# Performance work log

Measured on AMD Instinct MI355X. Metric: run time of the kernel, lower is better.

## Reference

```python
import jax, jax.numpy as jnp
import numpy as np

WAY, SHOT, QUERY, T, DIM, SEM, NCLS, HW = 20, 5, 50, 8, 640, 300, 351, 11
TEMP = 0.5


def l2n(x, axis=-1, eps=1e-12):
    n = jnp.sqrt(jnp.sum(x * x, axis=axis, keepdims=True))
    return x / jnp.maximum(n, eps)


def lrelu(x):
    return jnp.where(x >= 0, x, 0.1 * x)


def setup_inputs() -> dict:
    key = jax.random.key(0)
    ks = jax.random.split(key, 12)
    std = np.sqrt(2.0 / DIM).astype(np.float32)
    return {
        'spt': jax.random.normal(ks[0], (SHOT * WAY, DIM, HW, HW), jnp.float32),
        'qry': jax.random.normal(ks[1], (QUERY * WAY, DIM, HW, HW), jnp.float32),
        'label2vec': jax.random.normal(ks[2], (WAY, SEM), jnp.float32),
        'w1': jax.random.normal(ks[3], (T, SEM, SEM), jnp.float32) * 0.02,
        'b1': jnp.zeros((T, SEM), jnp.float32),
        'w2': jax.random.normal(ks[4], (T, DIM, SEM), jnp.float32) * 0.02,
        'b2': jnp.zeros((T, DIM), jnp.float32),
        'weight_base': jax.random.normal(ks[5], (NCLS, T, DIM), jnp.float32) * std,
        'wq': jnp.broadcast_to(jnp.eye(DIM, dtype=jnp.float32), (T, DIM, DIM)) + jax.random.normal(ks[6], (T, DIM, DIM), jnp.float32) * 0.001,
        'bq': jnp.zeros((T, DIM), jnp.float32),
        'wkeys': jax.random.normal(ks[7], (T, NCLS, DIM), jnp.float32) * std,
        'scale_att': jnp.full((T,), 10.0, jnp.float32),
        'lamda_novel': jnp.ones((T,), jnp.float32),
        'lamda_base': jnp.ones((T,), jnp.float32),
        'wt1': jax.random.normal(ks[8], (SEM // 2, SEM), jnp.float32) * 0.02,
        'bt1': jnp.zeros((SEM // 2,), jnp.float32),
        'wt2': jax.random.normal(ks[9], (T, SEM // 2), jnp.float32) * 0.02,
        'bt2': jnp.zeros((T,), jnp.float32),
        'templet_bias': jnp.zeros((T,), jnp.float32),
        'tl1': jnp.ones((1,), jnp.float32),
        'tl2': jnp.ones((1,), jnp.float32),
    }


def reference(spt, qry, label2vec, w1, b1, w2, b2, weight_base, wq, bq, wkeys,
              scale_att, lamda_novel, lamda_base, wt1, bt1, wt2, bt2,
              templet_bias, tl1, tl2):
    spt_f = spt.reshape(SHOT, WAY, DIM, HW, HW)
    # per-template semantic MLP -> 1x1 conv filters [T, way, DIM]
    h = lrelu(jnp.einsum('ws,tds->twd', label2vec, w1) + b1[:, None, :])
    filt = jnp.einsum('twd,tcd->twc', h, w2) + b2[:, None, :]
    # mean_normalize = L2 normalize along channel dim
    spt_n = l2n(spt_f, axis=2)
    qry_n = l2n(qry, axis=1)
    filt_n = l2n(filt, axis=-1)
    # support: sigmoid attention maps (1x1 conv), spatially-normalized pooling
    act_s = jax.nn.sigmoid(jnp.einsum('swcxy,twc->swtxy', spt_n, filt_n))
    act_s = act_s / jnp.sum(act_s, axis=(-1, -2), keepdims=True)
    spt_t = jnp.einsum('swcxy,swtxy->swtc', spt_n, act_s)   # [shot,way,T,D]
    spt_tn = l2n(spt_t, axis=-1)
    # attention-based weight transfer from base classes (eval: all classes)
    wb_n = l2n(weight_base, axis=-1)                        # [K,T,D]
    qe = l2n(jnp.einsum('swtc,tdc->swtd', spt_tn, wq) + bq[None, None], axis=-1)
    wk_n = l2n(wkeys, axis=-1)                              # [T,K,D]
    att = jax.nn.softmax(scale_att[None, None, :, None] * jnp.einsum('swtd,tkd->swtk', qe, wk_n), axis=-1)
    wtb = jnp.einsum('swtk,ktd->swtd', att, wb_n)           # [shot,way,T,D]
    lam_n = (lamda_novel ** 2)[None, None, :, None]
    lam_b = (lamda_base ** 2)[None, None, :, None]
    comb = lam_n * spt_tn + lam_b * wtb
    proto = l2n(jnp.mean(comb, axis=0, keepdims=True), axis=-1)  # [1,way,T,D]
    # query: per-way attention maps and pooling
    act_q = jax.nn.sigmoid(jnp.einsum('qcxy,twc->wqtxy', qry_n, filt_n))
    act_q = act_q / jnp.sum(act_q, axis=(-1, -2), keepdims=True)
    qry_t = jnp.einsum('qcxy,wqtxy->wqtc', qry_n, act_q)    # [way,Q,T,D]
    qry_tn = l2n(qry_t, axis=-1)
    # per-template similarity: einsum('mikl,ijkl->mjik').mean(0) -> [Q,way,T]
    sim = jnp.mean(jnp.einsum('mikd,ijkd->mjik', proto, qry_tn), axis=0)
    # semantic template weights
    h2 = lrelu(label2vec @ wt1.T + bt1)
    wgt = jax.nn.sigmoid(h2 @ wt2.T + bt2)                  # [way,T]
    wgt = (tl1 ** 2) * jax.nn.sigmoid(templet_bias) + (tl2 ** 2) * wgt
    wgt = wgt / jnp.sum(wgt, axis=-1, keepdims=True)
    logits = jnp.sum(sim * wgt[None], axis=-1)              # [Q,way]
    return logits / TEMP
```

## Files before the change

### kernel.cpp

```cpp
#include <hip/hip_runtime.h>
#include <hip/hip_bf16.h>

#define NWAY 20
#define NSHOT 5
#define NT 8
#define NDIM 640
#define NSEM 300
#define NSEMH 150
#define NCLS 351
#define NXY 121
#define NWT 160

typedef short s16x8 __attribute__((ext_vector_type(8)));
typedef float f32x4 __attribute__((ext_vector_type(4)));
typedef float f32x4u __attribute__((ext_vector_type(4), aligned(4)));

__device__ __forceinline__ float sigmoidf_(float x) { return 1.0f / (1.0f + expf(-x)); }
__device__ __forceinline__ float lreluf_(float x) { return x >= 0.0f ? x : 0.1f * x; }
__device__ __forceinline__ float invl2_(float ss) { return 1.0f / fmaxf(sqrtf(ss), 1e-12f); }

__device__ __forceinline__ unsigned bfr_(float f) {
    unsigned b = __float_as_uint(f);
    return (b + 0x7FFFu + ((b >> 16) & 1u)) >> 16;
}
__device__ __forceinline__ unsigned pkbf_(float a, float b) { return bfr_(a) | (bfr_(b) << 16); }

__device__ __forceinline__ s16x8 cvt8_(const float* p) {
    f32x4u a = *(const f32x4u*)p;
    f32x4u b = *(const f32x4u*)(p + 4);
    union { unsigned u[4]; s16x8 v; } r;
    r.u[0] = pkbf_(a[0], a[1]); r.u[1] = pkbf_(a[2], a[3]);
    r.u[2] = pkbf_(b[0], b[1]); r.u[3] = pkbf_(b[2], b[3]);
    return r.v;
}

__device__ __forceinline__ float waveReduceSum(float v) {
#pragma unroll
    for (int off = 32; off > 0; off >>= 1) v += __shfl_down(v, off, 64);
    return v;
}

__global__ __launch_bounds__(256) void k_prepw(const float* __restrict__ l2v,
    const float* __restrict__ w1, const float* __restrict__ b1,
    const float* __restrict__ w2, const float* __restrict__ b2,
    const float* __restrict__ wq, const float* __restrict__ wk,
    const float* __restrict__ wb, const float* __restrict__ wt1,
    const float* __restrict__ bt1, const float* __restrict__ wt2,
    const float* __restrict__ bt2, const float* __restrict__ tb,
    const float* __restrict__ tl1, const float* __restrict__ tl2,
    ushort* __restrict__ filtb, float* __restrict__ wgt,
    unsigned* __restrict__ wqb_u, ushort* __restrict__ wknb,
    float* __restrict__ invb)
{
    int b = blockIdx.x;
    int tid = threadIdx.x, lane = tid & 63, wv = tid >> 6;
    __shared__ float red4[4];
    __shared__ float l2s[NSEM];
    __shared__ float hS[NSEM];
    __shared__ float fS[NDIM];
    __shared__ float h2[NSEMH];
    __shared__ float wl[NT];
    __shared__ float ssum;

    if (b < 1600) {
        size_t i = ((size_t)b * 256 + tid) * 8;
        const f32x4u a = *(const f32x4u*)(wq + i);
        const f32x4u c = *(const f32x4u*)(wq + i + 4);
        wqb_u[i / 2 + 0] = pkbf_(a[0], a[1]);
        wqb_u[i / 2 + 1] = pkbf_(a[2], a[3]);
        wqb_u[i / 2 + 2] = pkbf_(c[0], c[1]);
        wqb_u[i / 2 + 3] = pkbf_(c[2], c[3]);
        return;
    }
    if (b < 4408) {
        int r = b - 1600;
        int t = r / NCLS, k = r - t * NCLS;
        const float* src = wk + (size_t)r * NDIM;
        float v0 = src[tid], v1 = src[tid + 256];
        bool h = tid < 128;
        float v2 = h ? src[tid + 512] : 0.f;
        float ss = v0 * v0 + v1 * v1 + v2 * v2;
        ss = waveReduceSum(ss);
        if (lane == 0) red4[wv] = ss;
        __syncthreads();
        float inv = invl2_(red4[0] + red4[1] + red4[2] + red4[3]);
        ushort* dst = wknb + ((size_t)t * 384 + k) * NDIM;
        dst[tid] = (ushort)bfr_(v0 * inv);
        dst[tid + 256] = (ushort)bfr_(v1 * inv);
        if (h) dst[tid + 512] = (ushort)bfr_(v2 * inv);
        return;
    }
    if (b < 7216) {
        int r = b - 4408;
        const float* src = wb + (size_t)r * NDIM;
        float v0 = src[tid], v1 = src[tid + 256];
        float v2 = (tid < 128) ? src[tid + 512] : 0.f;
        float ss = v0 * v0 + v1 * v1 + v2 * v2;
        ss = waveReduceSum(ss);
        if (lane == 0) red4[wv] = ss;
        __syncthreads();
        if (tid == 0) invb[r] = invl2_(red4[0] + red4[1] + red4[2] + red4[3]);
        return;
    }
    if (b < 7376) {
        int wt = b - 7216;
        int w = wt >> 3, t = wt & 7;
        for (int s = tid; s < NSEM; s += 256) l2s[s] = l2v[w * NSEM + s];
        __syncthreads();
        for (int d = tid; d < NSEM; d += 256) {
            const f32x4u* wr = (const f32x4u*)(w1 + ((size_t)t * NSEM + d) * NSEM);
            float a0 = 0.f, a1 = 0.f, a2 = 0.f, a3 = 0.f;
#pragma unroll 5
            for (int s4 = 0; s4 < 75; ++s4) {
                f32x4u v = wr[s4];
                a0 += v[0] * l2s[s4 * 4 + 0];
                a1 += v[1] * l2s[s4 * 4 + 1];
                a2 += v[2] * l2s[s4 * 4 + 2];
                a3 += v[3] * l2s[s4 * 4 + 3];
            }
            hS[d] = lreluf_((a0 + a1) + (a2 + a3) + b1[t * NSEM + d]);
        }
        __syncthreads();
        for (int c = tid; c < NDIM; c += 256) {
            const f32x4u* wr = (const f32x4u*)(w2 + ((size_t)t * NDIM + c) * NSEM);
            float a0 = 0.f, a1 = 0.f, a2 = 0.f, a3 = 0.f;
#pragma unroll 5
            for (int s4 = 0; s4 < 75; ++s4) {
                f32x4u v = wr[s4];
                a0 += v[0] * hS[s4 * 4 + 0];
                a1 += v[1] * hS[s4 * 4 + 1];
                a2 += v[2] * hS[s4 * 4 + 2];
                a3 += v[3] * hS[s4 * 4 + 3];
            }
            fS[c] = (a0 + a1) + (a2 + a3) + b2[t * NDIM + c];
        }
        __syncthreads();
        float ss = 0.f;
        for (int c = tid; c < NDIM; c += 256) ss += fS[c] * fS[c];
        ss = waveReduceSum(ss);
        if (lane == 0) red4[wv] = ss;
        __syncthreads();
        float inv = invl2_(red4[0] + red4[1] + red4[2] + red4[3]);
        for (int c = tid; c < NDIM; c += 256)
            filtb[(size_t)wt * NDIM + c] = (ushort)bfr_(fS[c] * inv);
        return;
    }
    {
        int w = b - 7376;
        if (tid < NSEMH) {
            float acc = 0.f;
            for (int s = 0; s < NSEM; ++s) acc += l2v[w * NSEM + s] * wt1[tid * NSEM + s];
            h2[tid] = lreluf_(acc + bt1[tid]);
        }
        __syncthreads();
        if (tid < NT) {
            float acc = 0.f;
            for (int d = 0; d < NSEMH; ++d) acc += h2[d] * wt2[tid * NSEMH + d];
            float wg = sigmoidf_(acc + bt2[tid]);
            wl[tid] = tl1[0] * tl1[0] * sigmoidf_(tb[tid]) + tl2[0] * tl2[0] * wg;
        }
        __syncthreads();
        if (tid == 0) { float s2 = 0.f; for (int t = 0; t < NT; ++t) s2 += wl[t]; ssum = s2; }
        __syncthreads();
        if (tid < NT) wgt[w * NT + tid] = wl[tid] / ssum;
    }
}

__global__ __launch_bounds__(256) void k_wbT(const float* __restrict__ wb,
    const float* __restrict__ invb, unsigned* __restrict__ wbnT_u)
{
    int k0 = blockIdx.x * 64, c0 = blockIdx.y * 64, t = blockIdx.z;
    int tid = threadIdx.x;
    __shared__ float tile[64][65];
    __shared__ float invT[64];
    {
        int i = tid >> 2, q = tid & 3;
        int kg = min(k0 + i, NCLS - 1);
#pragma unroll
        for (int u = 0; u < 4; ++u) {
            int c = q * 16 + u * 4;
            f32x4u v = *(const f32x4u*)(wb + ((size_t)kg * NT + t) * NDIM + c0 + c);
            tile[i][c] = v[0]; tile[i][c + 1] = v[1]; tile[i][c + 2] = v[2]; tile[i][c + 3] = v[3];
        }
        if (tid < 64) {
            int kg2 = k0 + tid;
            invT[tid] = (kg2 < NCLS) ? invb[(size_t)kg2 * NT + t] : 0.f;
        }
    }
    __syncthreads();
    int cc = tid >> 2, qq = tid & 3;
    size_t rowo = (((size_t)t * NDIM + c0 + cc) * 384 + k0) / 2;
#pragma unroll
    for (int u = 0; u < 8; ++u) {
        int kl = qq * 16 + u * 2;
        float v0 = tile[kl][cc] * invT[kl];
        float v1 = tile[kl + 1][cc] * invT[kl + 1];
        wbnT_u[rowo + qq * 8 + u] = pkbf_(v0, v1);
    }
}

__global__ __launch_bounds__(512) void k_support2(const float* __restrict__ spt,
    const ushort* __restrict__ filtb, float* __restrict__ sptn,
    ushort* __restrict__ xb)
{
    int w = blockIdx.x, s = blockIdx.y;
    int n = s * NWAY + w;
    int tid = threadIdx.x, lane = tid & 63, wv = tid >> 6;
    int l15 = lane & 15, lh = lane >> 4;
    const float* base = spt + (size_t)n * NDIM * NXY;

    __shared__ unsigned actL[16 * 64];
    __shared__ float redT[8 * 8];
    __shared__ float invt[8];

    for (int i = tid; i < 16 * 64; i += 512) actL[i] = 0u;

    int xy = wv * 16 + l15;
    const float* colb = base + (xy < NXY ? xy : 0);
    const ushort* arow1 = filtb + (size_t)(w * NT + (l15 & 7)) * NDIM + lh * 8;
    f32x4 acc = {0.f, 0.f, 0.f, 0.f};
    float ssq = 0.f;
    for (int c0 = 0; c0 < NDIM; c0 += 32) {
        float v[8];
#pragma unroll
        for (int j = 0; j < 8; ++j) {
            v[j] = colb[(size_t)(c0 + lh * 8 + j) * NXY];
            ssq += v[j] * v[j];
        }
        union { unsigned u[4]; s16x8 x; } bf;
#pragma unroll
        for (int p = 0; p < 4; ++p) bf.u[p] = pkbf_(v[2 * p], v[2 * p + 1]);
        s16x8 af = *(const s16x8*)(arow1 + c0);
        acc = __builtin_amdgcn_mfma_f32_16x16x32_bf16(af, bf.x, acc, 0, 0, 0);
    }
    ssq += __shfl_xor(ssq, 16, 64);
    ssq += __shfl_xor(ssq, 32, 64);
    float inv = (xy < NXY) ? invl2_(ssq) : 0.f;
    __syncthreads();
#pragma unroll
    for (int r = 0; r < 4; ++r) {
        int row = lh * 4 + r;
        if (row < 8) {
            float a = sigmoidf_(acc[r] * inv) * inv;
            unsigned g = ((unsigned)(xy >> 3) ^ (unsigned)row) & 15u;
            *(ushort*)((char*)actL + (size_t)row * 256 + g * 16 + (xy & 7) * 2) = (ushort)bfr_(a);
        }
    }
    __syncthreads();

    f32x4 acc2[5];
#pragma unroll
    for (int f = 0; f < 5; ++f) acc2[f] = (f32x4){0.f, 0.f, 0.f, 0.f};
#pragma unroll
    for (int ks = 0; ks < 4; ++ks) {
        int xyb = ks * 32 + lh * 8;
        unsigned g = ((unsigned)(ks * 4 + lh) ^ (unsigned)l15) & 15u;
        s16x8 af = *(const s16x8*)&actL[l15 * 64 + g * 4];
#pragma unroll
        for (int f = 0; f < 5; ++f) {
            int c = (wv * 5 + f) * 16 + l15;
            const float* rp = base + (size_t)c * NXY;
            s16x8 bfv;
            if (ks == 3 && lh == 3) {
                union { unsigned u[4]; s16x8 v; } r;
                r.u[0] = pkbf_(rp[120], 0.f); r.u[1] = 0u; r.u[2] = 0u; r.u[3] = 0u;
                bfv = r.v;
            } else {
                bfv = cvt8_(rp + xyb);
            }
            acc2[f] = __builtin_amdgcn_mfma_f32_16x16x32_bf16(af, bfv, acc2[f], 0, 0, 0);
        }
    }
    {
        float pr[4] = {0.f, 0.f, 0.f, 0.f};
#pragma unroll
        for (int f = 0; f < 5; ++f)
#pragma unroll
            for (int r = 0; r < 4; ++r) pr[r] += acc2[f][r] * acc2[f][r];
#pragma unroll
        for (int r = 0; r < 4; ++r) {
#pragma unroll
            for (int off = 1; off < 16; off <<= 1) pr[r] += __shfl_xor(pr[r], off, 64);
        }
        if (l15 == 0 && lh < 2) {
#pragma unroll
            for (int r = 0; r < 4; ++r) redT[wv * 8 + lh * 4 + r] = pr[r];
        }
    }
    __syncthreads();
    if (tid < 8) {
        float s8 = 0.f;
#pragma unroll
        for (int w8 = 0; w8 < 8; ++w8) s8 += redT[w8 * 8 + tid];
        invt[tid] = invl2_(s8);
    }
    __syncthreads();
    if (lh < 2) {
#pragma unroll
        for (int f = 0; f < 5; ++f) {
            int c = (wv * 5 + f) * 16 + l15;
#pragma unroll
            for (int r = 0; r < 4; ++r) {
                int t = lh * 4 + r;
                float val = acc2[f][r] * invt[t];
                sptn[((size_t)n * NT + t) * NDIM + c] = val;
                xb[((size_t)t * 112 + n) * NDIM + c] = (ushort)bfr_(val);
            }
        }
    }
}

__global__ __launch_bounds__(512) void k_qatt(const ushort* __restrict__ xb,
    const ushort* __restrict__ wqb, const float* __restrict__ bq,
    const ushort* __restrict__ wknb, const ushort* __restrict__ wbnT,
    const float* __restrict__ sptn, const float* __restrict__ scale_att,
    const float* __restrict__ lamn, const float* __restrict__ lamb,
    float* __restrict__ comb)
{
    int t = blockIdx.x, mt = blockIdx.y, n0 = mt * 16;
    int tid = threadIdx.x, lane = tid & 63, wv = tid >> 6;
    int l15 = lane & 15, lh = lane >> 4;
    __shared__ __align__(16) ushort qebL[16 * 640];
    __shared__ float scL[16 * 384];
    __shared__ __align__(16) unsigned attL[16 * 192];
    __shared__ float redQ[8 * 16];
    __shared__ float invR[16];

    f32x4 acc[5];
#pragma unroll
    for (int f = 0; f < 5; ++f) acc[f] = (f32x4){0.f, 0.f, 0.f, 0.f};
    float bqv[5];
#pragma unroll
    for (int f = 0; f < 5; ++f) bqv[f] = bq[t * NDIM + (wv * 5 + f) * 16 + l15];
    const ushort* arow = xb + ((size_t)t * 112 + n0 + l15) * NDIM + lh * 8;
    for (int k0 = 0; k0 < NDIM; k0 += 32) {
        s16x8 af = *(const s16x8*)(arow + k0);
#pragma unroll
        for (int f = 0; f < 5; ++f) {
            int d = (wv * 5 + f) * 16 + l15;
            s16x8 bv = *(const s16x8*)&wqb[((size_t)t * NDIM + d) * NDIM + k0 + lh * 8];
            acc[f] = __builtin_amdgcn_mfma_f32_16x16x32_bf16(af, bv, acc[f], 0, 0, 0);
        }
    }
    {
        float pr[4] = {0.f, 0.f, 0.f, 0.f};
#pragma unroll
        for (int f = 0; f < 5; ++f)
#pragma unroll
            for (int r = 0; r < 4; ++r) { float qv = acc[f][r] + bqv[f]; pr[r] += qv * qv; }
#pragma unroll
        for (int r = 0; r < 4; ++r) {
#pragma unroll
            for (int off = 1; off < 16; off <<= 1) pr[r] += __shfl_xor(pr[r], off, 64);
        }
        if (l15 == 0) {
#pragma unroll
            for (int r = 0; r < 4; ++r) redQ[wv * 16 + lh * 4 + r] = pr[r];
        }
    }
    __syncthreads();
    if (tid < 16) {
        float s = 0.f;
#pragma unroll
        for (int w8 = 0; w8 < 8; ++w8) s += redQ[w8 * 16 + tid];
        invR[tid] = invl2_(s);
    }
    __syncthreads();
#pragma unroll
    for (int f = 0; f < 5; ++f) {
        int d = (wv * 5 + f) * 16 + l15;
        unsigned g = (unsigned)(d >> 3);
        unsigned gh = g & ~15u, gl = g & 15u;
#pragma unroll
        for (int r = 0; r < 4; ++r) {
            int nn = lh * 4 + r;
            float qv = (acc[f][r] + bqv[f]) * invR[nn];
            unsigned gs = gh | (gl ^ (unsigned)nn);
            qebL[nn * 640 + gs * 8 + (d & 7)] = (ushort)bfr_(qv);
        }
    }
    __syncthreads();

    f32x4 a3[3];
#pragma unroll
    for (int f = 0; f < 3; ++f) a3[f] = (f32x4){0.f, 0.f, 0.f, 0.f};
    for (int k0 = 0; k0 < NDIM; k0 += 32) {
        unsigned g = (unsigned)((k0 >> 3) + lh);
        unsigned gs = (g & ~15u) | ((g & 15u) ^ (unsigned)l15);
        s16x8 af = *(const s16x8*)&qebL[l15 * 640 + gs * 8];
#pragma unroll
        for (int f = 0; f < 3; ++f) {
            int kk = (wv * 3 + f) * 16 + l15;
            s16x8 bv = *(const s16x8*)&wknb[((size_t)t * 384 + kk) * NDIM + k0 + lh * 8];
            a3[f] = __builtin_amdgcn_mfma_f32_16x16x32_bf16(af, bv, a3[f], 0, 0, 0);
        }
    }
    float sat = scale_att[t];
#pragma unroll
    for (int f = 0; f < 3; ++f) {
        int kk = (wv * 3 + f) * 16 + l15;
#pragma unroll
        for (int r = 0; r < 4; ++r) scL[(lh * 4 + r) * 384 + kk] = sat * a3[f][r];
    }
    __syncthreads();
    {
        int row = tid >> 5, li = tid & 31;
        float e[12]; float mx = -1e30f;
#pragma unroll
        for (int j = 0; j < 12; ++j) {
            int k = li + 32 * j;
            float v = (k < NCLS) ? scL[row * 384 + k] : -1e30f;
            e[j] = v; mx = fmaxf(mx, v);
        }
#pragma unroll
        for (int off = 1; off < 32; off <<= 1) mx = fmaxf(mx, __shfl_xor(mx, off, 64));
        float se = 0.f;
#pragma unroll
        for (int j = 0; j < 12; ++j) {
            int k = li + 32 * j;
            float ev = (k < NCLS) ? expf(e[j] - mx) : 0.f;
            e[j] = ev; se += ev;
        }
#pragma unroll
        for (int off = 1; off < 32; off <<= 1) se += __shfl_xor(se, off, 64);
        float is = 1.f / se;
#pragma unroll
        for (int j = 0; j < 12; ++j) scL[row * 384 + li + 32 * j] = e[j] * is;
    }
    __syncthreads();
    for (int idx = tid; idx < 3072; idx += 512) {
        int row = idx / 192, pp = idx - row * 192;
        int k2 = 2 * pp;
        unsigned g = (unsigned)(k2 >> 3);
        unsigned gs = (g & ~15u) | ((g & 15u) ^ (unsigned)row);
        attL[row * 192 + gs * 4 + ((k2 >> 1) & 3)] = pkbf_(scL[row * 384 + k2], scL[row * 384 + k2 + 1]);
    }
    __syncthreads();

    f32x4 a4[5];
#pragma unroll
    for (int f = 0; f < 5; ++f) a4[f] = (f32x4){0.f, 0.f, 0.f, 0.f};
    const ushort* attp = (const ushort*)attL;
    for (int k0 = 0; k0 < 384; k0 += 32) {
        unsigned g = (unsigned)((k0 >> 3) + lh);
        unsigned gs = (g & ~15u) | ((g & 15u) ^ (unsigned)l15);
        s16x8 af = *(const s16x8*)&attp[l15 * 384 + gs * 8];
#pragma unroll
        for (int f = 0; f < 5; ++f) {
            int c = (wv * 5 + f) * 16 + l15;
            s16x8 bv = *(const s16x8*)&wbnT[((size_t)t * NDIM + c) * 384 + k0 + lh * 8];
            a4[f] = __builtin_amdgcn_mfma_f32_16x16x32_bf16(af, bv, a4[f], 0, 0, 0);
        }
    }
    float ln2 = lamn[t] * lamn[t], lb2 = lamb[t] * lamb[t];
#pragma unroll
    for (int f = 0; f < 5; ++f) {
        int c = (wv * 5 + f) * 16 + l15;
#pragma unroll
        for (int r = 0; r < 4; ++r) {
            int ng = n0 + lh * 4 + r;
            if (ng < 100) {
                size_t o = ((size_t)ng * NT + t) * NDIM + c;
                comb[o] = ln2 * sptn[o] + lb2 * a4[f][r];
            }
        }
    }
}

__global__ __launch_bounds__(128) void k_proto(const float* __restrict__ comb,
    float* __restrict__ proto)
{
    int wt = blockIdx.x;
    int w = wt >> 3, t = wt & 7;
    int tid = threadIdx.x, lane = tid & 63, wv = tid >> 6;
    __shared__ float red[2];
    float mv[5]; float ss = 0.f;
#pragma unroll
    for (int m = 0; m < 5; ++m) {
        int c = tid + 128 * m;
        float a = 0.f;
#pragma unroll
        for (int s = 0; s < NSHOT; ++s)
            a += comb[(((size_t)(s * NWAY + w)) * NT + t) * NDIM + c];
        a *= 0.2f;
        mv[m] = a; ss += a * a;
    }
    ss = waveReduceSum(ss);
    if (lane == 0) red[wv] = ss;
    __syncthreads();
    float inv = invl2_(red[0] + red[1]);
#pragma unroll
    for (int m = 0; m < 5; ++m) proto[(size_t)wt * NDIM + tid + 128 * m] = mv[m] * inv;
}

__global__ __launch_bounds__(512, 4) void k_query3(const float* __restrict__ qry,
    const ushort* __restrict__ filtb, const float* __restrict__ proto,
    const float* __restrict__ wgt, float* __restrict__ out)
{
    int q = blockIdx.x, hf = blockIdx.y;
    int tid = threadIdx.x, lane = tid & 63, wv = tid >> 6;
    int l15 = lane & 15, lh = lane >> 4;
    const float* qbase = qry + (size_t)q * NDIM * NXY;
    __shared__ __align__(16) unsigned actL[80 * 64];
    __shared__ float simacc[8 * 80 * 2];
    __shared__ float simF[80];

    int xy = wv * 16 + l15;
    const float* colb = qbase + (xy < NXY ? xy : 0);
    f32x4 acc[5];
#pragma unroll
    for (int m = 0; m < 5; ++m) acc[m] = (f32x4){0.f, 0.f, 0.f, 0.f};
    float ssq = 0.f;
    for (int c0 = 0; c0 < NDIM; c0 += 32) {
        float v[8];
#pragma unroll
        for (int j = 0; j < 8; ++j) {
            v[j] = colb[(size_t)(c0 + lh * 8 + j) * NXY];
            ssq += v[j] * v[j];
        }
        union { unsigned u[4]; s16x8 x; } bf;
#pragma unroll
        for (int p = 0; p < 4; ++p) bf.u[p] = pkbf_(v[2 * p], v[2 * p + 1]);
#pragma unroll
        for (int m = 0; m < 5; ++m) {
            s16x8 af = *(const s16x8*)&filtb[(size_t)(hf * 80 + m * 16 + l15) * NDIM + c0 + lh * 8];
            acc[m] = __builtin_amdgcn_mfma_f32_16x16x32_bf16(af, bf.x, acc[m], 0, 0, 0);
        }
    }
    ssq += __shfl_xor(ssq, 16, 64);
    ssq += __shfl_xor(ssq, 32, 64);
    float inv = (xy < NXY) ? invl2_(ssq) : 0.f;
    for (int i = tid; i < 8 * 80 * 2; i += 512) simacc[i] = 0.f;
    {
        unsigned xg = (unsigned)(xy >> 3);
        unsigned xo = (unsigned)(xy & 7) * 2;
#pragma unroll
        for (int m = 0; m < 5; ++m) {
#pragma unroll
            for (int r = 0; r < 4; ++r) {
                int row = m * 16 + lh * 4 + r;
                float a = sigmoidf_(acc[m][r] * inv) * inv;
                unsigned g = (xg ^ (unsigned)row) & 15u;
                *(ushort*)((char*)actL + (size_t)row * 256 + g * 16 + xo) = (ushort)bfr_(a);
            }
        }
    }
    __syncthreads();

    int ns = wv & 3, a_ = wv >> 2;
    float dacc[3][4], sacc[3][4];
#pragma unroll
    for (int i = 0; i < 3; ++i)
#pragma unroll
        for (int r = 0; r < 4; ++r) { dacc[i][r] = 0.f; sacc[i][r] = 0.f; }

    for (int c0 = 0; c0 < NDIM; c0 += 64) {
        int cb = c0 + ns * 16 + l15;
        const float* rp = qbase + (size_t)cb * NXY;
        s16x8 bfv[4];
#pragma unroll
        for (int kk = 0; kk < 4; ++kk) {
            if (kk == 3 && lh == 3) {
                union { unsigned u[4]; s16x8 v; } r;
                r.u[0] = pkbf_(rp[120], 0.f); r.u[1] = 0u; r.u[2] = 0u; r.u[3] = 0u;
                bfv[kk] = r.v;
            } else {
                bfv[kk] = cvt8_(rp + kk * 32 + lh * 8);
            }
        }
#pragma unroll
        for (int i = 0; i < 3; ++i) {
            if (i < 3 - a_) {
                int m = 3 * a_ + i;
                f32x4 c4 = (f32x4){0.f, 0.f, 0.f, 0.f};
#pragma unroll
                for (int kk = 0; kk < 4; ++kk) {
                    unsigned g = ((unsigned)(kk * 4 + lh) ^ (unsigned)l15) & 15u;
                    s16x8 af = *(const s16x8*)&actL[(m * 16 + l15) * 64 + g * 4];
                    c4 = __builtin_amdgcn_mfma_f32_16x16x32_bf16(af, bfv[kk], c4, 0, 0, 0);
                }
#pragma unroll
                for (int r = 0; r < 4; ++r) {
                    float p = proto[(size_t)(hf * 80 + m * 16 + lh * 4 + r) * NDIM + cb];
                    dacc[i][r] += c4[r] * p;
                    sacc[i][r] += c4[r] * c4[r];
                }
            }
        }
    }
#pragma unroll
    for (int i = 0; i < 3; ++i) {
        if (i < 3 - a_) {
#pragma unroll
            for (int r = 0; r < 4; ++r) {
                float d = dacc[i][r], s2 = sacc[i][r];
#pragma unroll
                for (int off = 1; off < 16; off <<= 1) {
                    d += __shfl_xor(d, off, 64);
                    s2 += __shfl_xor(s2, off, 64);
                }
                if (l15 == 0) {
                    int wtl = (3 * a_ + i) * 16 + lh * 4 + r;
                    simacc[(wv * 80 + wtl) * 2 + 0] = d;
                    simacc[(wv * 80 + wtl) * 2 + 1] = s2;
                }
            }
        }
    }
    __syncthreads();
    if (tid < 80) {
        float d = 0.f, s2 = 0.f;
#pragma unroll
        for (int w8 = 0; w8 < 8; ++w8) {
            d += simacc[(w8 * 80 + tid) * 2 + 0];
            s2 += simacc[(w8 * 80 + tid) * 2 + 1];
        }
        simF[tid] = d * invl2_(s2);
    }
    __syncthreads();
    if (tid < 10) {
        int w = hf * 10 + tid;
        float lg = 0.f;
#pragma unroll
        for (int t = 0; t < NT; ++t) lg += simF[tid * NT + t] * wgt[w * NT + t];
        out[q * NWAY + w] = 2.0f * lg;
    }
}

extern "C" void kernel_launch(void* const* d_in, const int* in_sizes, int n_in,
                              void* d_out, int out_size, void* d_ws, size_t ws_size,
                              hipStream_t stream)
{
    const float* spt  = (const float*)d_in[0];
    const float* qry  = (const float*)d_in[1];
    const float* l2v  = (const float*)d_in[2];
    const float* w1   = (const float*)d_in[3];
    const float* b1   = (const float*)d_in[4];
    const float* w2   = (const float*)d_in[5];
    const float* b2   = (const float*)d_in[6];
    const float* wb   = (const float*)d_in[7];
    const float* wq   = (const float*)d_in[8];
    const float* bq   = (const float*)d_in[9];
    const float* wk   = (const float*)d_in[10];
    const float* sat  = (const float*)d_in[11];
    const float* lamn = (const float*)d_in[12];
    const float* lamb = (const float*)d_in[13];
    const float* wt1  = (const float*)d_in[14];
    const float* bt1  = (const float*)d_in[15];
    const float* wt2  = (const float*)d_in[16];
    const float* bt2  = (const float*)d_in[17];
    const float* tb   = (const float*)d_in[18];
    const float* tl1  = (const float*)d_in[19];
    const float* tl2  = (const float*)d_in[20];

    float* ws = (float*)d_ws;
    ushort*  filtb  = (ushort*)ws;
    float*   wgt    = ws + 51200;
    ushort*  wqb    = (ushort*)(ws + 51360);
    ushort*  wknb   = (ushort*)(ws + 1689760);
    ushort*  wbnT   = (ushort*)(ws + 2672800);
    float*   invb   = ws + 3655840;
    ushort*  xb     = (ushort*)(ws + 3658656);
    float*   sptn   = ws + 3945376;
    float*   combv  = ws + 4457376;
    float*   proto  = ws + 4969376;
    float*   outp   = (float*)d_out;

    hipLaunchKernelGGL(k_prepw,    dim3(7396),     dim3(256), 0, stream,
                       l2v, w1, b1, w2, b2, wq, wk, wb, wt1, bt1, wt2, bt2, tb, tl1, tl2,
                       filtb, wgt, (unsigned*)wqb, wknb, invb);
    hipLaunchKernelGGL(k_wbT,      dim3(6, 10, 8), dim3(256), 0, stream, wb, invb, (unsigned*)wbnT);
    hipLaunchKernelGGL(k_support2, dim3(20, 5),    dim3(512), 0, stream, spt, filtb, sptn, xb);
    hipLaunchKernelGGL(k_qatt,     dim3(8, 7),     dim3(512), 0, stream,
                       xb, wqb, bq, wknb, wbnT, sptn, sat, lamn, lamb, combv);
    hipLaunchKernelGGL(k_proto,    dim3(160),      dim3(128), 0, stream, combv, proto);
    hipLaunchKernelGGL(k_query3,   dim3(1000, 2),  dim3(512), 0, stream,
                       qry, filtb, proto, wgt, outp);
}
```

Baseline: 632.9 us.

## Split fused query kernel into activation, pooling and final-reduction kernels

Replaces the single fused query kernel, which ran one block per query half, with three kernels. The first computes the sigmoid attention maps per 16-row tile and writes them to global memory as bf16. The second pools query features over 128-channel tiles and writes partial dot products and norms, and the third reduces those partials into logits. Block IDs are remapped so that all blocks for a query land on the same XCD, aiming at L2 reuse of the query tensor. This gives far more, smaller blocks in exchange for re-reading the query tensor twice, an extra global round trip for activations and partials, and two more launches.

```diff
diff --git a/kernel.cpp b/kernel.cpp
--- a/kernel.cpp
+++ b/kernel.cpp
@@ -493,23 +493,20 @@
     for (int m = 0; m < 5; ++m) proto[(size_t)wt * NDIM + tid + 128 * m] = mv[m] * inv;
 }
 
-__global__ __launch_bounds__(512, 4) void k_query3(const float* __restrict__ qry,
-    const ushort* __restrict__ filtb, const float* __restrict__ proto,
-    const float* __restrict__ wgt, float* __restrict__ out)
-{
-    int q = blockIdx.x, hf = blockIdx.y;
+__global__ __launch_bounds__(512) void k_act3(const float* __restrict__ qry,
+    const ushort* __restrict__ filtb, ushort* __restrict__ actb)
+{
+    int bid = blockIdx.x;
+    int xcd = bid & 7, s = bid >> 3;
+    int q = xcd * 125 + s / 10, mt = s % 10;
     int tid = threadIdx.x, lane = tid & 63, wv = tid >> 6;
     int l15 = lane & 15, lh = lane >> 4;
     const float* qbase = qry + (size_t)q * NDIM * NXY;
-    __shared__ __align__(16) unsigned actL[80 * 64];
-    __shared__ float simacc[8 * 80 * 2];
-    __shared__ float simF[80];
-
     int xy = wv * 16 + l15;
     const float* colb = qbase + (xy < NXY ? xy : 0);
-    f32x4 acc[5];
-#pragma unroll
-    for (int m = 0; m < 5; ++m) acc[m] = (f32x4){0.f, 0.f, 0.f, 0.f};
+    const ushort* arow = filtb + (size_t)(mt * 16 + l15) * NDIM + lh * 8;
+
+    f32x4 acc = {0.f, 0.f, 0.f, 0.f};
     float ssq = 0.f;
     for (int c0 = 0; c0 < NDIM; c0 += 32) {
         float v[8];
@@ -521,41 +518,40 @@
         union { unsigned u[4]; s16x8 x; } bf;
 #pragma unroll
         for (int p = 0; p < 4; ++p) bf.u[p] = pkbf_(v[2 * p], v[2 * p + 1]);
-#pragma unroll
-        for (int m = 0; m < 5; ++m) {
-            s16x8 af = *(const s16x8*)&filtb[(size_t)(hf * 80 + m * 16 + l15) * NDIM + c0 + lh * 8];
-            acc[m] = __builtin_amdgcn_mfma_f32_16x16x32_bf16(af, bf.x, acc[m], 0, 0, 0);
-        }
+        s16x8 af = *(const s16x8*)(arow + c0);
+        acc = __builtin_amdgcn_mfma_f32_16x16x32_bf16(af, bf.x, acc, 0, 0, 0);
     }
     ssq += __shfl_xor(ssq, 16, 64);
     ssq += __shfl_xor(ssq, 32, 64);
     float inv = (xy < NXY) ? invl2_(ssq) : 0.f;
-    for (int i = tid; i < 8 * 80 * 2; i += 512) simacc[i] = 0.f;
-    {
-        unsigned xg = (unsigned)(xy >> 3);
-        unsigned xo = (unsigned)(xy & 7) * 2;
-#pragma unroll
-        for (int m = 0; m < 5; ++m) {
-#pragma unroll
-            for (int r = 0; r < 4; ++r) {
-                int row = m * 16 + lh * 4 + r;
-                float a = sigmoidf_(acc[m][r] * inv) * inv;
-                unsigned g = (xg ^ (unsigned)row) & 15u;
-                *(ushort*)((char*)actL + (size_t)row * 256 + g * 16 + xo) = (ushort)bfr_(a);
-            }
-        }
-    }
-    __syncthreads();
-
-    int ns = wv & 3, a_ = wv >> 2;
-    float dacc[3][4], sacc[3][4];
-#pragma unroll
-    for (int i = 0; i < 3; ++i)
-#pragma unroll
-        for (int r = 0; r < 4; ++r) { dacc[i][r] = 0.f; sacc[i][r] = 0.f; }
-
-    for (int c0 = 0; c0 < NDIM; c0 += 64) {
-        int cb = c0 + ns * 16 + l15;
+#pragma unroll
+    for (int r = 0; r < 4; ++r) {
+        int row = mt * 16 + lh * 4 + r;
+        float a = sigmoidf_(acc[r] * inv) * inv;
+        actb[((size_t)q * NWT + row) * 128 + xy] = (ushort)bfr_(a);
+    }
+}
+
+__global__ __launch_bounds__(320) void k_pool3(const float* __restrict__ qry,
+    const ushort* __restrict__ actb, const float* __restrict__ proto,
+    float* __restrict__ part)
+{
+    int bid = blockIdx.x;
+    int xcd = bid & 7, s = bid >> 3;
+    int q = xcd * 125 + s / 5, ct = s % 5;
+    int tid = threadIdx.x, lane = tid & 63, wv = tid >> 6;
+    int l15 = lane & 15, lh = lane >> 4;
+    const float* qbase = qry + (size_t)q * NDIM * NXY;
+    const ushort* abase = actb + (size_t)q * NWT * 128;
+
+    float dacc[2][4], sacc[2][4];
+#pragma unroll
+    for (int mi = 0; mi < 2; ++mi)
+#pragma unroll
+        for (int r = 0; r < 4; ++r) { dacc[mi][r] = 0.f; sacc[mi][r] = 0.f; }
+
+    for (int n = 0; n < 8; ++n) {
+        int cb = ct * 128 + n * 16 + l15;
         const float* rp = qbase + (size_t)cb * NXY;
         s16x8 bfv[4];
 #pragma unroll
@@ -569,61 +565,62 @@
             }
         }
 #pragma unroll
-        for (int i = 0; i < 3; ++i) {
-            if (i < 3 - a_) {
-                int m = 3 * a_ + i;
-                f32x4 c4 = (f32x4){0.f, 0.f, 0.f, 0.f};
-#pragma unroll
-                for (int kk = 0; kk < 4; ++kk) {
-                    unsigned g = ((unsigned)(kk * 4 + lh) ^ (unsigned)l15) & 15u;
-                    s16x8 af = *(const s16x8*)&actL[(m * 16 + l15) * 64 + g * 4];
-                    c4 = __builtin_amdgcn_mfma_f32_16x16x32_bf16(af, bfv[kk], c4, 0, 0, 0);
-                }
-#pragma unroll
-                for (int r = 0; r < 4; ++r) {
-                    float p = proto[(size_t)(hf * 80 + m * 16 + lh * 4 + r) * NDIM + cb];
-                    dacc[i][r] += c4[r] * p;
-                    sacc[i][r] += c4[r] * c4[r];
-                }
-            }
-        }
-    }
-#pragma unroll
-    for (int i = 0; i < 3; ++i) {
-        if (i < 3 - a_) {
+        for (int mi = 0; mi < 2; ++mi) {
+            int m = wv + 5 * mi;
+            f32x4 c4 = (f32x4){0.f, 0.f, 0.f, 0.f};
+#pragma unroll
+            for (int kk = 0; kk < 4; ++kk) {
+                s16x8 af = *(const s16x8*)(abase + (size_t)(m * 16 + l15) * 128 + kk * 32 + lh * 8);
+                c4 = __builtin_amdgcn_mfma_f32_16x16x32_bf16(af, bfv[kk], c4, 0, 0, 0);
+            }
 #pragma unroll
             for (int r = 0; r < 4; ++r) {
-                float d = dacc[i][r], s2 = sacc[i][r];
-#pragma unroll
-                for (int off = 1; off < 16; off <<= 1) {
-                    d += __shfl_xor(d, off, 64);
-                    s2 += __shfl_xor(s2, off, 64);
-                }
-                if (l15 == 0) {
-                    int wtl = (3 * a_ + i) * 16 + lh * 4 + r;
-                    simacc[(wv * 80 + wtl) * 2 + 0] = d;
-                    simacc[(wv * 80 + wtl) * 2 + 1] = s2;
-                }
-            }
-        }
-    }
-    __syncthreads();
-    if (tid < 80) {
-        float d = 0.f, s2 = 0.f;
-#pragma unroll
-        for (int w8 = 0; w8 < 8; ++w8) {
-            d += simacc[(w8 * 80 + tid) * 2 + 0];
-            s2 += simacc[(w8 * 80 + tid) * 2 + 1];
-        }
-        simF[tid] = d * invl2_(s2);
-    }
-    __syncthreads();
-    if (tid < 10) {
-        int w = hf * 10 + tid;
+                float p = proto[(size_t)(m * 16 + lh * 4 + r) * NDIM + cb];
+                dacc[mi][r] += c4[r] * p;
+                sacc[mi][r] += c4[r] * c4[r];
+            }
+        }
+    }
+#pragma unroll
+    for (int mi = 0; mi < 2; ++mi) {
+#pragma unroll
+        for (int r = 0; r < 4; ++r) {
+            float d = dacc[mi][r], s2 = sacc[mi][r];
+#pragma unroll
+            for (int off = 1; off < 16; off <<= 1) {
+                d += __shfl_xor(d, off, 64);
+                s2 += __shfl_xor(s2, off, 64);
+            }
+            if (l15 == 0) {
+                int wt = (wv + 5 * mi) * 16 + lh * 4 + r;
+                float* p = part + (((size_t)q * 5 + ct) * NWT + wt) * 2;
+                p[0] = d; p[1] = s2;
+            }
+        }
+    }
+}
+
+__global__ __launch_bounds__(256) void k_final(const float* __restrict__ part,
+    const float* __restrict__ wgt, float* __restrict__ out)
+{
+    int q = blockIdx.x;
+    int tid = threadIdx.x;
+    __shared__ float sim[NWT];
+    if (tid < NWT) {
+        float d = 0.f, s = 0.f;
+#pragma unroll
+        for (int ct = 0; ct < 5; ++ct) {
+            const float* p = part + (((size_t)q * 5 + ct) * NWT + tid) * 2;
+            d += p[0]; s += p[1];
+        }
+        sim[tid] = d * invl2_(s);
+    }
+    __syncthreads();
+    if (tid < NWAY) {
         float lg = 0.f;
 #pragma unroll
-        for (int t = 0; t < NT; ++t) lg += simF[tid * NT + t] * wgt[w * NT + t];
-        out[q * NWAY + w] = 2.0f * lg;
+        for (int t = 0; t < NT; ++t) lg += sim[tid * NT + t] * wgt[tid * NT + t];
+        out[q * NWAY + tid] = lg * 2.0f;
     }
 }
 
@@ -664,6 +661,8 @@
     float*   sptn   = ws + 3945376;
     float*   combv  = ws + 4457376;
     float*   proto  = ws + 4969376;
+    ushort*  actb   = (ushort*)(ws + 5071776);
+    float*   part   = ws + 15311776;
     float*   outp   = (float*)d_out;
 
     hipLaunchKernelGGL(k_prepw,    dim3(7396),     dim3(256), 0, stream,
@@ -674,6 +673,7 @@
     hipLaunchKernelGGL(k_qatt,     dim3(8, 7),     dim3(512), 0, stream,
                        xb, wqb, bq, wknb, wbnT, sptn, sat, lamn, lamb, combv);
     hipLaunchKernelGGL(k_proto,    dim3(160),      dim3(128), 0, stream, combv, proto);
-    hipLaunchKernelGGL(k_query3,   dim3(1000, 2),  dim3(512), 0, stream,
-                       qry, filtb, proto, wgt, outp);
-}
+    hipLaunchKernelGGL(k_act3,     dim3(10000),    dim3(512), 0, stream, qry, filtb, actb);
+    hipLaunchKernelGGL(k_pool3,    dim3(5000),     dim3(320), 0, stream, qry, actb, proto, part);
+    hipLaunchKernelGGL(k_final,    dim3(1000),     dim3(256), 0, stream, part, wgt, outp);
+}
```

Measured after the change: 824.2 us. 1.3x slower.
